# Kernel optimization log

Hardware: AMD Instinct MI355X
Metric: run time of the kernel (lower is better)

## Reference

```python
import jax, jax.numpy as jnp
import numpy as np

N = 500_000   # total nodes
D = 256       # in_dim
G = 1024      # num graphs (segments)
H = max(32, D // 2)  # gate hidden = 128
L = D // 2    # local pool dim = 128


def setup_inputs() -> dict:
    key = jax.random.key(0)
    ks = jax.random.split(key, 8)
    x = jax.random.normal(ks[0], (N, D), dtype=jnp.float32)
    batch = jnp.sort(jax.random.randint(ks[1], (N,), 0, G, dtype=jnp.int32))
    s = 0.02
    w1 = jax.random.normal(ks[2], (D, H), dtype=jnp.float32) * s
    b1 = jnp.zeros((H,), dtype=jnp.float32)
    w2 = jax.random.normal(ks[3], (H, 1), dtype=jnp.float32) * s
    b2 = jnp.zeros((1,), dtype=jnp.float32)
    lp_w = jax.random.normal(ks[4], (D, L), dtype=jnp.float32) * s
    lp_b = jnp.zeros((L,), dtype=jnp.float32)
    return {"x": x, "batch": batch, "w1": w1, "b1": b1, "w2": w2,
            "b2": b2, "lp_w": lp_w, "lp_b": lp_b}


def reference(x, batch, w1, b1, w2, b2, lp_w, lp_b):
    # segment counts (guard empty segments)
    ones = jnp.ones((x.shape[0],), dtype=x.dtype)
    cnt = jax.ops.segment_sum(ones, batch, num_segments=G)
    cnt = jnp.maximum(cnt, 1.0)[:, None]                      # [G,1]

    # mean pool
    mean_p = jax.ops.segment_sum(x, batch, num_segments=G) / cnt

    # max pool
    max_p = jax.ops.segment_max(x, batch, num_segments=G)

    # global attention pool: gate MLP -> per-segment softmax -> weighted sum
    # (Dropout is identity at inference.)
    h = jax.nn.gelu(x @ w1 + b1, approximate=False)           # [N,H]
    gate = (h @ w2 + b2)[:, 0]                                # [N]
    gmax = jax.ops.segment_max(gate, batch, num_segments=G)   # [G]
    e = jnp.exp(gate - gmax[batch])                           # [N]
    denom = jax.ops.segment_sum(e, batch, num_segments=G)     # [G]
    a = e / denom[batch]                                      # [N] softmax per graph
    att_p = jax.ops.segment_sum(a[:, None] * x, batch, num_segments=G)

    # local MLP pool then mean
    local = jax.nn.gelu(x @ lp_w + lp_b, approximate=False)   # [N,L]
    local_mean = jax.ops.segment_sum(local, batch, num_segments=G) / cnt

    return jnp.concatenate([mean_p, max_p, att_p, local_mean], axis=-1)  # [G, 3D + D//2]
```

## Files before the change

kernel.cpp:

```cpp
#include <hip/hip_runtime.h>
#include <hip/hip_bf16.h>
#include <float.h>
#include <math.h>


typedef __bf16 bf16;
typedef __bf16 bf16x4 __attribute__((ext_vector_type(4)));
typedef __bf16 bf16x8 __attribute__((ext_vector_type(8)));
typedef float f32x4 __attribute__((ext_vector_type(4)));

#define D 256
#define HDIM 128
#define LDIM 128
#define ROWS 48
#define XCOL 264
#define NMT 3
#define SPLIT 4

__device__ __forceinline__ float gelu_f(float v) {
    return 0.5f * v * (1.0f + erff(v * 0.70710678118654752f));
}

__global__ __launch_bounds__(256) void k_prep(const float* __restrict__ w1,
                                              const float* __restrict__ lpw,
                                              bf16* __restrict__ w1T,
                                              bf16* __restrict__ lpT) {
    int t = blockIdx.x * 256 + threadIdx.x;
    if (t < HDIM * D) {
        int n = t >> 8;
        int k = t & 255;
        w1T[t] = (bf16)w1[k * HDIM + n];
        lpT[t] = (bf16)lpw[k * LDIM + n];
    }
}

__global__ __launch_bounds__(256) void k_bounds(const int* __restrict__ batch,
                                                int* __restrict__ segstart,
                                                int N, int G) {
    int i = blockIdx.x * 256 + threadIdx.x;
    if (i >= N) return;
    int b = batch[i];
    if (i == 0) {
        for (int g = 0; g <= b; ++g) segstart[g] = 0;
    } else {
        int p = batch[i - 1];
        for (int g = p + 1; g <= b; ++g) segstart[g] = i;
    }
    if (i == N - 1) {
        for (int g = b + 1; g <= G; ++g) segstart[g] = N;
    }
}

__global__ __launch_bounds__(256) __attribute__((amdgpu_waves_per_eu(3, 3)))
void k_fused(const float* __restrict__ x, const int* __restrict__ segstart,
             const bf16* __restrict__ w1T, const float* __restrict__ b1,
             const float* __restrict__ w2, const float* __restrict__ b2,
             const bf16* __restrict__ lpT, const float* __restrict__ lpb,
             float* __restrict__ psum, float* __restrict__ pmax,
             float* __restrict__ patt, float* __restrict__ pls,
             float* __restrict__ pscal)
{
    __shared__ bf16  xs[ROWS][XCOL];
    __shared__ float gpart[4][64];
    __shared__ float red[3][4][256];

    const int blk  = blockIdx.x;
    const int g    = blk >> 2;
    const int part = blk & 3;
    const int tid  = threadIdx.x;
    const int wave = tid >> 6;
    const int lane = tid & 63;
    const int quad = lane >> 4;
    const int l16  = lane & 15;

    const int gs = segstart[g], ge = segstart[g + 1];
    const int cnt = ge - gs;
    const int per = (cnt + SPLIT - 1) >> 2;
    const int start = gs + part * per;
    const int end   = min(start + per, ge);

    const int c0 = wave * 32 + l16;
    const int c1 = c0 + 16;
    const float b1c0 = b1[c0], b1c1 = b1[c1];
    const float w2c0 = w2[c0], w2c1 = w2[c1];
    const float lb0  = lpb[c0], lb1 = lpb[c1];
    const float b2c  = b2[0];
    const bf16* wb0 = w1T + c0 * D;
    const bf16* wb1 = w1T + c1 * D;
    const bf16* pb0 = lpT + c0 * D;
    const bf16* pb1 = lpT + c1 * D;

    float msum0=0.f, msum1=0.f, msum2=0.f, msum3=0.f;
    float mmax0=-FLT_MAX, mmax1=-FLT_MAX, mmax2=-FLT_MAX, mmax3=-FLT_MAX;
    float asum0=0.f, asum1=0.f, asum2=0.f, asum3=0.f;
    float ls0=0.f, ls1=0.f;
    float m_run = -FLT_MAX, denom = 0.f;

    const f32x4 zf = {0.f, 0.f, 0.f, 0.f};

    for (int base = start; base < end; base += ROWS) {
        const int vr = min(ROWS, end - base);
        const float* xb = x + (long)base * D + (lane << 2);

        float4 xr[12];
        if (vr == ROWS) {
            #pragma unroll
            for (int it = 0; it < 12; ++it)
                xr[it] = *(const float4*)(xb + (it * 4 + wave) * D);
            #pragma unroll
            for (int it = 0; it < 12; ++it) {
                msum0 += xr[it].x; msum1 += xr[it].y;
                msum2 += xr[it].z; msum3 += xr[it].w;
                mmax0 = fmaxf(mmax0, xr[it].x); mmax1 = fmaxf(mmax1, xr[it].y);
                mmax2 = fmaxf(mmax2, xr[it].z); mmax3 = fmaxf(mmax3, xr[it].w);
            }
        } else {
            #pragma unroll
            for (int it = 0; it < 12; ++it) {
                const int row = it * 4 + wave;
                xr[it] = make_float4(0.f, 0.f, 0.f, 0.f);
                if (row < vr) xr[it] = *(const float4*)(xb + row * D);
            }
            #pragma unroll
            for (int it = 0; it < 12; ++it) {
                if (it * 4 + wave < vr) {
                    msum0 += xr[it].x; msum1 += xr[it].y;
                    msum2 += xr[it].z; msum3 += xr[it].w;
                    mmax0 = fmaxf(mmax0, xr[it].x); mmax1 = fmaxf(mmax1, xr[it].y);
                    mmax2 = fmaxf(mmax2, xr[it].z); mmax3 = fmaxf(mmax3, xr[it].w);
                }
            }
        }
        #pragma unroll
        for (int it = 0; it < 12; ++it) {
            bf16x4 pk;
            pk[0] = (bf16)xr[it].x; pk[1] = (bf16)xr[it].y;
            pk[2] = (bf16)xr[it].z; pk[3] = (bf16)xr[it].w;
            *(bf16x4*)(&xs[it * 4 + wave][lane << 2]) = pk;
        }
        __syncthreads();

        f32x4 h0[NMT], h1[NMT], l0[NMT], l1[NMT];
        #pragma unroll
        for (int mt = 0; mt < NMT; ++mt) { h0[mt]=zf; h1[mt]=zf; l0[mt]=zf; l1[mt]=zf; }

        #pragma unroll
        for (int kt = 0; kt < 8; ++kt) {
            const int k0 = kt * 32 + quad * 8;
            const bf16x8 bw0 = *(const bf16x8*)(wb0 + k0);
            const bf16x8 bw1 = *(const bf16x8*)(wb1 + k0);
            const bf16x8 bp0 = *(const bf16x8*)(pb0 + k0);
            const bf16x8 bp1 = *(const bf16x8*)(pb1 + k0);
            #pragma unroll
            for (int mt = 0; mt < NMT; ++mt) {
                const bf16x8 a = *(const bf16x8*)(&xs[mt * 16 + l16][k0]);
                h0[mt] = __builtin_amdgcn_mfma_f32_16x16x32_bf16(a, bw0, h0[mt], 0, 0, 0);
                h1[mt] = __builtin_amdgcn_mfma_f32_16x16x32_bf16(a, bw1, h1[mt], 0, 0, 0);
                l0[mt] = __builtin_amdgcn_mfma_f32_16x16x32_bf16(a, bp0, l0[mt], 0, 0, 0);
                l1[mt] = __builtin_amdgcn_mfma_f32_16x16x32_bf16(a, bp1, l1[mt], 0, 0, 0);
            }
        }

        #pragma unroll
        for (int mt = 0; mt < NMT; ++mt) {
            #pragma unroll
            for (int r = 0; r < 4; ++r) {
                float v = gelu_f(h0[mt][r] + b1c0) * w2c0
                        + gelu_f(h1[mt][r] + b1c1) * w2c1;
                v += __shfl_down(v, 8, 16);
                v += __shfl_down(v, 4, 16);
                v += __shfl_down(v, 2, 16);
                v += __shfl_down(v, 1, 16);
                if (l16 == 0) gpart[wave][mt * 16 + quad * 4 + r] = v;
            }
        }
        __syncthreads();

        float gv = -FLT_MAX;
        if (lane < vr)
            gv = gpart[0][lane] + gpart[1][lane] + gpart[2][lane] + gpart[3][lane] + b2c;
        float cm = gv;
        #pragma unroll
        for (int off = 32; off > 0; off >>= 1) cm = fmaxf(cm, __shfl_xor(cm, off));
        const float m_new = fmaxf(m_run, cm);
        const float fr = expf(m_run - m_new);
        const float ew = (lane < vr) ? expf(gv - m_new) : 0.f;
        float se = ew;
        #pragma unroll
        for (int off = 32; off > 0; off >>= 1) se += __shfl_xor(se, off);
        denom = denom * fr + se;
        m_run = m_new;

        if (vr == ROWS) {
            #pragma unroll
            for (int mt = 0; mt < NMT; ++mt)
                #pragma unroll
                for (int r = 0; r < 4; ++r) {
                    ls0 += gelu_f(l0[mt][r] + lb0);
                    ls1 += gelu_f(l1[mt][r] + lb1);
                }
        } else {
            #pragma unroll
            for (int mt = 0; mt < NMT; ++mt)
                #pragma unroll
                for (int r = 0; r < 4; ++r) {
                    if (mt * 16 + quad * 4 + r < vr) {
                        ls0 += gelu_f(l0[mt][r] + lb0);
                        ls1 += gelu_f(l1[mt][r] + lb1);
                    }
                }
        }

        asum0 *= fr; asum1 *= fr; asum2 *= fr; asum3 *= fr;
        #pragma unroll
        for (int it = 0; it < 12; ++it) {
            const float e = __shfl(ew, it * 4 + wave);
            asum0 += e * xr[it].x; asum1 += e * xr[it].y;
            asum2 += e * xr[it].z; asum3 += e * xr[it].w;
        }
    }

    ls0 += __shfl_xor(ls0, 16); ls0 += __shfl_xor(ls0, 32);
    ls1 += __shfl_xor(ls1, 16); ls1 += __shfl_xor(ls1, 32);

    f32x4 v0 = {msum0, msum1, msum2, msum3};
    f32x4 v1 = {mmax0, mmax1, mmax2, mmax3};
    f32x4 v2 = {asum0, asum1, asum2, asum3};
    *(f32x4*)(&red[0][wave][lane << 2]) = v0;
    *(f32x4*)(&red[1][wave][lane << 2]) = v1;
    *(f32x4*)(&red[2][wave][lane << 2]) = v2;
    if (quad == 0) {
        pls[(long)blk * LDIM + c0] = ls0;
        pls[(long)blk * LDIM + c1] = ls1;
    }
    if (tid == 0) {
        const int pcnt = (end > start) ? (end - start) : 0;
        pscal[(long)blk * 4 + 0] = m_run;
        pscal[(long)blk * 4 + 1] = denom;
        pscal[(long)blk * 4 + 2] = (float)pcnt;
    }
    __syncthreads();
    {
        const int col = tid;
        const float s  = red[0][0][col] + red[0][1][col] + red[0][2][col] + red[0][3][col];
        const float mx = fmaxf(fmaxf(red[1][0][col], red[1][1][col]),
                               fmaxf(red[1][2][col], red[1][3][col]));
        const float a  = red[2][0][col] + red[2][1][col] + red[2][2][col] + red[2][3][col];
        psum[(long)blk * 256 + col] = s;
        pmax[(long)blk * 256 + col] = mx;
        patt[(long)blk * 256 + col] = a;
    }
}

__global__ __launch_bounds__(256) void k_merge(
    const float* __restrict__ psum, const float* __restrict__ pmax,
    const float* __restrict__ patt, const float* __restrict__ pls,
    const float* __restrict__ pscal, float* __restrict__ out)
{
    const int g   = blockIdx.x;
    const int tid = threadIdx.x;
    __shared__ float sm[SPLIT], sd[SPLIT], sc[SPLIT];
    if (tid < SPLIT) {
        sm[tid] = pscal[(long)(g * SPLIT + tid) * 4 + 0];
        sd[tid] = pscal[(long)(g * SPLIT + tid) * 4 + 1];
        sc[tid] = pscal[(long)(g * SPLIT + tid) * 4 + 2];
    }
    __syncthreads();
    const float M   = fmaxf(fmaxf(sm[0], sm[1]), fmaxf(sm[2], sm[3]));
    const float cnt = sc[0] + sc[1] + sc[2] + sc[3];
    float w[SPLIT];
    float denom = 0.f;
    #pragma unroll
    for (int p = 0; p < SPLIT; ++p) {
        w[p] = expf(sm[p] - M);
        denom += sd[p] * w[p];
    }
    const float inv  = 1.0f / fmaxf(cnt, 1.0f);
    const float invd = (denom > 0.f) ? 1.0f / denom : 0.f;
    const long  o    = (long)g * 896;
    const long  pb   = (long)g * SPLIT * 256;
    {
        const int col = tid;
        float s = 0.f, a = 0.f, mx = -FLT_MAX;
        #pragma unroll
        for (int p = 0; p < SPLIT; ++p) {
            s += psum[pb + p * 256 + col];
            mx = fmaxf(mx, pmax[pb + p * 256 + col]);
            a += patt[pb + p * 256 + col] * w[p];
        }
        out[o + col]       = s * inv;
        out[o + 256 + col] = (cnt > 0.f) ? mx : -INFINITY;
        out[o + 512 + col] = a * invd;
    }
    if (tid < 128) {
        const long lb = (long)g * SPLIT * 128;
        float s = 0.f;
        #pragma unroll
        for (int p = 0; p < SPLIT; ++p) s += pls[lb + p * 128 + tid];
        out[o + 768 + tid] = s * inv;
    }
}

extern "C" void kernel_launch(void* const* d_in, const int* in_sizes, int n_in,
                              void* d_out, int out_size, void* d_ws, size_t ws_size,
                              hipStream_t stream) {
    const float* x   = (const float*)d_in[0];
    const int* batch = (const int*)d_in[1];
    const float* w1  = (const float*)d_in[2];
    const float* b1  = (const float*)d_in[3];
    const float* w2  = (const float*)d_in[4];
    const float* b2  = (const float*)d_in[5];
    const float* lpw = (const float*)d_in[6];
    const float* lpb = (const float*)d_in[7];
    float* out = (float*)d_out;

    const int N = in_sizes[0] / D;
    const int G = out_size / 896;
    const int NB = SPLIT * G;

    char* ws = (char*)d_ws;
    size_t off = 0;
    auto alloc = [&](size_t bytes) { void* p = ws + off; off = (off + bytes + 255) & ~(size_t)255; return p; };
    bf16*  w1T      = (bf16*)alloc((size_t)HDIM * D * sizeof(bf16));
    bf16*  lpT      = (bf16*)alloc((size_t)LDIM * D * sizeof(bf16));
    int*   segstart = (int*)alloc((size_t)(G + 1) * sizeof(int));
    float* psum     = (float*)alloc((size_t)NB * 256 * sizeof(float));
    float* pmax     = (float*)alloc((size_t)NB * 256 * sizeof(float));
    float* patt     = (float*)alloc((size_t)NB * 256 * sizeof(float));
    float* pls      = (float*)alloc((size_t)NB * 128 * sizeof(float));
    float* pscal    = (float*)alloc((size_t)NB * 4 * sizeof(float));

    k_prep<<<(HDIM * D + 255) / 256, 256, 0, stream>>>(w1, lpw, w1T, lpT);
    k_bounds<<<(N + 255) / 256, 256, 0, stream>>>(batch, segstart, N, G);
    k_fused<<<NB, 256, 0, stream>>>(x, segstart, w1T, b1, w2, b2, lpT, lpb,
                                    psum, pmax, patt, pls, pscal);
    k_merge<<<G, 256, 0, stream>>>(psum, pmax, patt, pls, pscal, out);
}
```

Before: 1.082 ms.

## Shrink row tile to 16 and stage x as fp32 in LDS

The rows processed per iteration drop from 48 to 16, and x tiles are now kept in LDS as fp32 instead of bf16 plus a 12-entry register array. The bf16 conversion moves into the MFMA k-loop, and the attention sum rereads x from LDS. The waves_per_eu cap is removed and the x buffer doubles as the final reduction scratch. The aim is to cut register and LDS pressure so more waves can run at once. In exchange there are more barriers per row, fewer global loads in flight per wave, and each wave repeats the A-operand conversion.

Result: no change. 1.067 ms (-1.4%).

```diff
diff --git a/kernel.cpp b/kernel.cpp
--- a/kernel.cpp
+++ b/kernel.cpp
@@ -5,16 +5,14 @@
 
 
 typedef __bf16 bf16;
-typedef __bf16 bf16x4 __attribute__((ext_vector_type(4)));
 typedef __bf16 bf16x8 __attribute__((ext_vector_type(8)));
 typedef float f32x4 __attribute__((ext_vector_type(4)));
 
 #define D 256
 #define HDIM 128
 #define LDIM 128
-#define ROWS 48
-#define XCOL 264
-#define NMT 3
+#define ROWS 16
+#define XPAD 260
 #define SPLIT 4
 
 __device__ __forceinline__ float gelu_f(float v) {
@@ -51,7 +49,7 @@
     }
 }
 
-__global__ __launch_bounds__(256) __attribute__((amdgpu_waves_per_eu(3, 3)))
+__global__ __launch_bounds__(256)
 void k_fused(const float* __restrict__ x, const int* __restrict__ segstart,
              const bf16* __restrict__ w1T, const float* __restrict__ b1,
              const float* __restrict__ w2, const float* __restrict__ b2,
@@ -60,9 +58,8 @@
              float* __restrict__ patt, float* __restrict__ pls,
              float* __restrict__ pscal)
 {
-    __shared__ bf16  xs[ROWS][XCOL];
-    __shared__ float gpart[4][64];
-    __shared__ float red[3][4][256];
+    __shared__ float xf[ROWS][XPAD];
+    __shared__ float gpart[4][16];
 
     const int blk  = blockIdx.x;
     const int g    = blk >> 2;
@@ -96,83 +93,68 @@
     float ls0=0.f, ls1=0.f;
     float m_run = -FLT_MAX, denom = 0.f;
 
-    const f32x4 zf = {0.f, 0.f, 0.f, 0.f};
-
     for (int base = start; base < end; base += ROWS) {
         const int vr = min(ROWS, end - base);
         const float* xb = x + (long)base * D + (lane << 2);
 
-        float4 xr[12];
         if (vr == ROWS) {
             #pragma unroll
-            for (int it = 0; it < 12; ++it)
-                xr[it] = *(const float4*)(xb + (it * 4 + wave) * D);
-            #pragma unroll
-            for (int it = 0; it < 12; ++it) {
-                msum0 += xr[it].x; msum1 += xr[it].y;
-                msum2 += xr[it].z; msum3 += xr[it].w;
-                mmax0 = fmaxf(mmax0, xr[it].x); mmax1 = fmaxf(mmax1, xr[it].y);
-                mmax2 = fmaxf(mmax2, xr[it].z); mmax3 = fmaxf(mmax3, xr[it].w);
+            for (int it = 0; it < 4; ++it) {
+                const int row = it * 4 + wave;
+                const float4 t4 = *(const float4*)(xb + row * D);
+                msum0 += t4.x; msum1 += t4.y; msum2 += t4.z; msum3 += t4.w;
+                mmax0 = fmaxf(mmax0, t4.x); mmax1 = fmaxf(mmax1, t4.y);
+                mmax2 = fmaxf(mmax2, t4.z); mmax3 = fmaxf(mmax3, t4.w);
+                f32x4 v; v[0]=t4.x; v[1]=t4.y; v[2]=t4.z; v[3]=t4.w;
+                *(f32x4*)(&xf[row][lane << 2]) = v;
             }
         } else {
             #pragma unroll
-            for (int it = 0; it < 12; ++it) {
+            for (int it = 0; it < 4; ++it) {
                 const int row = it * 4 + wave;
-                xr[it] = make_float4(0.f, 0.f, 0.f, 0.f);
-                if (row < vr) xr[it] = *(const float4*)(xb + row * D);
+                f32x4 v = {0.f, 0.f, 0.f, 0.f};
+                if (row < vr) {
+                    const float4 t4 = *(const float4*)(xb + row * D);
+                    msum0 += t4.x; msum1 += t4.y; msum2 += t4.z; msum3 += t4.w;
+                    mmax0 = fmaxf(mmax0, t4.x); mmax1 = fmaxf(mmax1, t4.y);
+                    mmax2 = fmaxf(mmax2, t4.z); mmax3 = fmaxf(mmax3, t4.w);
+                    v[0]=t4.x; v[1]=t4.y; v[2]=t4.z; v[3]=t4.w;
+                }
+                *(f32x4*)(&xf[row][lane << 2]) = v;
             }
-            #pragma unroll
-            for (int it = 0; it < 12; ++it) {
-                if (it * 4 + wave < vr) {
-                    msum0 += xr[it].x; msum1 += xr[it].y;
-                    msum2 += xr[it].z; msum3 += xr[it].w;
-                    mmax0 = fmaxf(mmax0, xr[it].x); mmax1 = fmaxf(mmax1, xr[it].y);
-                    mmax2 = fmaxf(mmax2, xr[it].z); mmax3 = fmaxf(mmax3, xr[it].w);
-                }
-            }
-        }
-        #pragma unroll
-        for (int it = 0; it < 12; ++it) {
-            bf16x4 pk;
-            pk[0] = (bf16)xr[it].x; pk[1] = (bf16)xr[it].y;
-            pk[2] = (bf16)xr[it].z; pk[3] = (bf16)xr[it].w;
-            *(bf16x4*)(&xs[it * 4 + wave][lane << 2]) = pk;
         }
         __syncthreads();
 
-        f32x4 h0[NMT], h1[NMT], l0[NMT], l1[NMT];
-        #pragma unroll
-        for (int mt = 0; mt < NMT; ++mt) { h0[mt]=zf; h1[mt]=zf; l0[mt]=zf; l1[mt]=zf; }
-
-        #pragma unroll
+        const f32x4 zf = {0.f, 0.f, 0.f, 0.f};
+        f32x4 h0 = zf, h1 = zf, l0 = zf, l1 = zf;
+        #pragma unroll 1
         for (int kt = 0; kt < 8; ++kt) {
             const int k0 = kt * 32 + quad * 8;
-            const bf16x8 bw0 = *(const bf16x8*)(wb0 + k0);
-            const bf16x8 bw1 = *(const bf16x8*)(wb1 + k0);
-            const bf16x8 bp0 = *(const bf16x8*)(pb0 + k0);
-            const bf16x8 bp1 = *(const bf16x8*)(pb1 + k0);
-            #pragma unroll
-            for (int mt = 0; mt < NMT; ++mt) {
-                const bf16x8 a = *(const bf16x8*)(&xs[mt * 16 + l16][k0]);
-                h0[mt] = __builtin_amdgcn_mfma_f32_16x16x32_bf16(a, bw0, h0[mt], 0, 0, 0);
-                h1[mt] = __builtin_amdgcn_mfma_f32_16x16x32_bf16(a, bw1, h1[mt], 0, 0, 0);
-                l0[mt] = __builtin_amdgcn_mfma_f32_16x16x32_bf16(a, bp0, l0[mt], 0, 0, 0);
-                l1[mt] = __builtin_amdgcn_mfma_f32_16x16x32_bf16(a, bp1, l1[mt], 0, 0, 0);
-            }
-        }
-
-        #pragma unroll
-        for (int mt = 0; mt < NMT; ++mt) {
-            #pragma unroll
-            for (int r = 0; r < 4; ++r) {
-                float v = gelu_f(h0[mt][r] + b1c0) * w2c0
-                        + gelu_f(h1[mt][r] + b1c1) * w2c1;
-                v += __shfl_down(v, 8, 16);
-                v += __shfl_down(v, 4, 16);
-                v += __shfl_down(v, 2, 16);
-                v += __shfl_down(v, 1, 16);
-                if (l16 == 0) gpart[wave][mt * 16 + quad * 4 + r] = v;
-            }
+            const bf16x8 bw0v = *(const bf16x8*)(wb0 + k0);
+            const bf16x8 bw1v = *(const bf16x8*)(wb1 + k0);
+            const bf16x8 bp0v = *(const bf16x8*)(pb0 + k0);
+            const bf16x8 bp1v = *(const bf16x8*)(pb1 + k0);
+            const float* xp = &xf[l16][k0];
+            const f32x4 fa = *(const f32x4*)(xp);
+            const f32x4 fb = *(const f32x4*)(xp + 4);
+            bf16x8 a;
+            a[0]=(bf16)fa[0]; a[1]=(bf16)fa[1]; a[2]=(bf16)fa[2]; a[3]=(bf16)fa[3];
+            a[4]=(bf16)fb[0]; a[5]=(bf16)fb[1]; a[6]=(bf16)fb[2]; a[7]=(bf16)fb[3];
+            h0 = __builtin_amdgcn_mfma_f32_16x16x32_bf16(a, bw0v, h0, 0, 0, 0);
+            h1 = __builtin_amdgcn_mfma_f32_16x16x32_bf16(a, bw1v, h1, 0, 0, 0);
+            l0 = __builtin_amdgcn_mfma_f32_16x16x32_bf16(a, bp0v, l0, 0, 0, 0);
+            l1 = __builtin_amdgcn_mfma_f32_16x16x32_bf16(a, bp1v, l1, 0, 0, 0);
+        }
+
+        #pragma unroll
+        for (int r = 0; r < 4; ++r) {
+            float v = gelu_f(h0[r] + b1c0) * w2c0
+                    + gelu_f(h1[r] + b1c1) * w2c1;
+            v += __shfl_down(v, 8, 16);
+            v += __shfl_down(v, 4, 16);
+            v += __shfl_down(v, 2, 16);
+            v += __shfl_down(v, 1, 16);
+            if (l16 == 0) gpart[wave][quad * 4 + r] = v;
         }
         __syncthreads();
 
@@ -191,44 +173,39 @@
         denom = denom * fr + se;
         m_run = m_new;
 
-        if (vr == ROWS) {
-            #pragma unroll
-            for (int mt = 0; mt < NMT; ++mt)
-                #pragma unroll
-                for (int r = 0; r < 4; ++r) {
-                    ls0 += gelu_f(l0[mt][r] + lb0);
-                    ls1 += gelu_f(l1[mt][r] + lb1);
-                }
-        } else {
-            #pragma unroll
-            for (int mt = 0; mt < NMT; ++mt)
-                #pragma unroll
-                for (int r = 0; r < 4; ++r) {
-                    if (mt * 16 + quad * 4 + r < vr) {
-                        ls0 += gelu_f(l0[mt][r] + lb0);
-                        ls1 += gelu_f(l1[mt][r] + lb1);
-                    }
-                }
+        #pragma unroll
+        for (int r = 0; r < 4; ++r) {
+            if (quad * 4 + r < vr) {
+                ls0 += gelu_f(l0[r] + lb0);
+                ls1 += gelu_f(l1[r] + lb1);
+            }
         }
 
         asum0 *= fr; asum1 *= fr; asum2 *= fr; asum3 *= fr;
         #pragma unroll
-        for (int it = 0; it < 12; ++it) {
-            const float e = __shfl(ew, it * 4 + wave);
-            asum0 += e * xr[it].x; asum1 += e * xr[it].y;
-            asum2 += e * xr[it].z; asum3 += e * xr[it].w;
-        }
+        for (int it = 0; it < 4; ++it) {
+            const int row = it * 4 + wave;
+            const float e = __shfl(ew, row);
+            const f32x4 v = *(const f32x4*)(&xf[row][lane << 2]);
+            asum0 += e * v[0]; asum1 += e * v[1];
+            asum2 += e * v[2]; asum3 += e * v[3];
+        }
+        __syncthreads();
     }
 
     ls0 += __shfl_xor(ls0, 16); ls0 += __shfl_xor(ls0, 32);
     ls1 += __shfl_xor(ls1, 16); ls1 += __shfl_xor(ls1, 32);
 
-    f32x4 v0 = {msum0, msum1, msum2, msum3};
-    f32x4 v1 = {mmax0, mmax1, mmax2, mmax3};
-    f32x4 v2 = {asum0, asum1, asum2, asum3};
-    *(f32x4*)(&red[0][wave][lane << 2]) = v0;
-    *(f32x4*)(&red[1][wave][lane << 2]) = v1;
-    *(f32x4*)(&red[2][wave][lane << 2]) = v2;
+    float* red = &xf[0][0];
+    const int cb = (wave << 8) + (lane << 2);
+    {
+        f32x4 v0 = {msum0, msum1, msum2, msum3};
+        f32x4 v1 = {asum0, asum1, asum2, asum3};
+        f32x4 v2 = {mmax0, mmax1, mmax2, mmax3};
+        *(f32x4*)(&red[cb])        = v0;
+        *(f32x4*)(&red[1024 + cb]) = v1;
+        *(f32x4*)(&red[2048 + cb]) = v2;
+    }
     if (quad == 0) {
         pls[(long)blk * LDIM + c0] = ls0;
         pls[(long)blk * LDIM + c1] = ls1;
@@ -242,13 +219,13 @@
     __syncthreads();
     {
         const int col = tid;
-        const float s  = red[0][0][col] + red[0][1][col] + red[0][2][col] + red[0][3][col];
-        const float mx = fmaxf(fmaxf(red[1][0][col], red[1][1][col]),
-                               fmaxf(red[1][2][col], red[1][3][col]));
-        const float a  = red[2][0][col] + red[2][1][col] + red[2][2][col] + red[2][3][col];
+        const float s  = red[col]        + red[256 + col]  + red[512 + col]  + red[768 + col];
+        const float a  = red[1024 + col] + red[1280 + col] + red[1536 + col] + red[1792 + col];
+        const float mx = fmaxf(fmaxf(red[2048 + col], red[2304 + col]),
+                               fmaxf(red[2560 + col], red[2816 + col]));
         psum[(long)blk * 256 + col] = s;
+        patt[(long)blk * 256 + col] = a;
         pmax[(long)blk * 256 + col] = mx;
-        patt[(long)blk * 256 + col] = a;
     }
 }
 
```
